# Kernel optimization log

Hardware: AMD Instinct MI355X
Metric: run time of the kernel (lower is better)

Reference implementation:

```python
import jax, jax.numpy as jnp
import numpy as np

B, F, T, K = 32, 256, 2048, 1024


def setup_inputs() -> dict:
    key = jax.random.key(0)
    k1, k2 = jax.random.split(key)
    x = jax.random.normal(k1, (B, F, T), dtype=jnp.float32)
    emb_weight = jax.random.normal(k2, (K, F), dtype=jnp.float32)
    return {"x": x, "emb_weight": emb_weight}


def reference(x, emb_weight):
    # x: [B, F, T] -> [B, T, F]
    xt = jnp.swapaxes(x, -1, -2)
    nf = xt.shape[-1]

    def sq_dist(a, c):
        # mean over feature dim of (a - c)^2, expanded to avoid a [B,T,K,F]
        # broadcast tensor: (|a|^2 - 2 a.c + |c|^2) / F -> [B, T, K]
        a2 = jnp.sum(a * a, axis=-1, keepdims=True)          # [B,T,1]
        c2 = jnp.sum(c * c, axis=-1)                          # [K]
        ac = jnp.einsum('btf,kf->btk', a, c)                  # [B,T,K]
        return (a2 - 2.0 * ac + c2) / nf

    w_sg = jax.lax.stop_gradient(emb_weight)
    x_sg = jax.lax.stop_gradient(xt)

    dist = sq_dist(xt, w_sg)                                  # [B,T,K]
    min_dist = jnp.min(dist, axis=-1)                         # [B,T]
    idxs = jnpp_argmin(dist) if False else jnp.argmin(dist, axis=-1)  # [B,T]

    loss_commit = min_dist.mean()                              # grads -> x only
    loss_codebook = jnp.min(sq_dist(x_sg, emb_weight), axis=-1).mean()  # grads -> codebook only

    out = w_sg[idxs]                                           # [B,T,F] gather (detached)
    out = jnp.swapaxes(out, -1, -2)                            # [B,F,T]
    return out, loss_commit, loss_codebook
```

## Files before the change

### kernel.cpp

```cpp
#include <hip/hip_runtime.h>

#define B_ 32
#define F_ 256
#define T_ 2048
#define K_ 1024
#define M_ (B_*T_)

#define MARGIN 0.45f
#define CAP 128

typedef _Float16 f16x8 __attribute__((ext_vector_type(8)));
typedef float f32x4 __attribute__((ext_vector_type(4)));

__global__ void k_prep(const float* __restrict__ emb, unsigned short* __restrict__ cprep,
                       double* __restrict__ c2d, float* __restrict__ c2f) {
    int k = blockIdx.x;
    int l = threadIdx.x;
    float4 v = *reinterpret_cast<const float4*>(emb + k * F_ + l * 4);
    union { _Float16 h[4]; unsigned long long ll; } cv;
    cv.h[0] = (_Float16)v.x; cv.h[1] = (_Float16)v.y;
    cv.h[2] = (_Float16)v.z; cv.h[3] = (_Float16)v.w;
    *reinterpret_cast<unsigned long long*>(cprep + k * F_ + l * 4) = cv.ll;
    double s = (double)v.x * v.x + (double)v.y * v.y
             + (double)v.z * v.z + (double)v.w * v.w;
    #pragma unroll
    for (int d = 1; d < 64; d <<= 1) s += __shfl_xor(s, d);
    if (l == 0) { c2d[k] = s; c2f[k] = (float)s; }
}

#define LOADB(dst, c2n, tt) {                                                    \
    const unsigned short* bp = cprep + ((tt) * 16 + row) * F_ + qd * 8;          \
    _Pragma("unroll")                                                            \
    for (int s_ = 0; s_ < 8; ++s_)                                               \
        dst[s_] = *reinterpret_cast<const f16x8*>(bp + s_ * 32);                 \
    c2n = c2f[(tt) * 16 + row];                                                  \
}

#define COMPUTE(bf, c2v, tt) {                                                   \
    const int kk = (tt) * 16 + row;                                              \
    f32x4 acc0 = {0.f, 0.f, 0.f, 0.f};                                           \
    f32x4 acc1 = {0.f, 0.f, 0.f, 0.f};                                           \
    _Pragma("unroll")                                                            \
    for (int s_ = 0; s_ < 8; ++s_) {                                             \
        acc0 = __builtin_amdgcn_mfma_f32_16x16x32_f16(ah0[s_], bf[s_], acc0, 0, 0, 0); \
        acc1 = __builtin_amdgcn_mfma_f32_16x16x32_f16(ah1[s_], bf[s_], acc1, 0, 0, 0); \
    }                                                                            \
    _Pragma("unroll")                                                            \
    for (int r_ = 0; r_ < 4; ++r_) {                                             \
        {                                                                        \
            float q = fmaf(acc0[r_], -2.0f, c2v + a2s[r_]);                      \
            int vi = (__float_as_int(q) & 0xFFFFFC00) | kk;                      \
            int t1 = max(m1i[r_], vi); m1i[r_] = min(m1i[r_], vi);               \
            int t2 = max(m2i[r_], t1); m2i[r_] = min(m2i[r_], t1);               \
            m3i[r_] = min(m3i[r_], t2);                                          \
        }                                                                        \
        {                                                                        \
            float q = fmaf(acc1[r_], -2.0f, c2v + a2s[4 + r_]);                  \
            int vi = (__float_as_int(q) & 0xFFFFFC00) | kk;                      \
            int t1 = max(m1i[4 + r_], vi); m1i[4 + r_] = min(m1i[4 + r_], vi);   \
            int t2 = max(m2i[4 + r_], t1); m2i[4 + r_] = min(m2i[4 + r_], t1);   \
            m3i[4 + r_] = min(m3i[4 + r_], t2);                                  \
        }                                                                        \
    }                                                                            \
}

__global__ __launch_bounds__(64, 2) void k_argmin(
    const float* __restrict__ x, const float* __restrict__ emb,
    const unsigned short* __restrict__ cprep,
    const double* __restrict__ c2d, const float* __restrict__ c2f,
    int* __restrict__ idx_out, double* __restrict__ partials)
{
    __shared__ int cand_cnt;
    __shared__ int cand_pk[CAP];
    __shared__ double cand_q[CAP];
    __shared__ int res_k[32];

    const int l = threadIdx.x;
    const int bid = blockIdx.x;
    const int b = bid >> 6;
    const int t0 = (bid & 63) * 32;
    const int row = l & 15;
    const int qd = l >> 4;

    if (l == 0) cand_cnt = 0;

    const float* xb = x + (size_t)b * (F_ * T_) + t0 + row + (size_t)qd * 8 * T_;
    float xsql = 0.f, xsqh = 0.f;
    f16x8 ah0[8], ah1[8];
    #pragma unroll
    for (int s = 0; s < 8; ++s) {
        #pragma unroll
        for (int j = 0; j < 8; ++j) {
            size_t fo = (size_t)(s * 32 + j) * T_;
            float v0 = xb[fo];
            float v1 = xb[fo + 16];
            ah0[s][j] = (_Float16)v0;
            ah1[s][j] = (_Float16)v1;
            xsql = fmaf(v0, v0, xsql);
            xsqh = fmaf(v1, v1, xsqh);
        }
    }
    float xl = xsql, xh = xsqh;
    xl += __shfl_xor(xl, 16); xl += __shfl_xor(xl, 32);
    xh += __shfl_xor(xh, 16); xh += __shfl_xor(xh, 32);
    float a2s[8];
    #pragma unroll
    for (int r = 0; r < 4; ++r) {
        a2s[r]     = __shfl(xl, qd * 4 + r);
        a2s[4 + r] = __shfl(xh, qd * 4 + r);
    }

    int m1i[8], m2i[8], m3i[8];
    #pragma unroll
    for (int i = 0; i < 8; ++i) { m1i[i] = 0x7FFFFFFF; m2i[i] = 0x7FFFFFFF; m3i[i] = 0x7FFFFFFF; }

    f16x8 bA[8], bB[8];
    float c2A, c2B;
    LOADB(bA, c2A, 0);
    #pragma unroll 1
    for (int t = 0; t < 64; t += 2) {
        LOADB(bB, c2B, t + 1);
        COMPUTE(bA, c2A, t);
        if (t + 2 < 64) LOADB(bA, c2A, t + 2);
        COMPUTE(bB, c2B, t + 1);
    }

    double loss_acc = 0.0;
    #pragma unroll
    for (int i = 0; i < 8; ++i) {
        int gm = m1i[i];
        #pragma unroll
        for (int d = 1; d < 16; d <<= 1) { int o = __shfl_xor(gm, d); gm = min(gm, o); }
        float thr = __int_as_float(gm & 0xFFFFFC00) + MARGIN;
        bool in1 = __int_as_float(m1i[i] & 0xFFFFFC00) <= thr;
        bool in2 = __int_as_float(m2i[i] & 0xFFFFFC00) <= thr;
        bool in3 = __int_as_float(m3i[i] & 0xFFFFFC00) <= thr;
        unsigned long long b1 = __ballot(in1), b2 = __ballot(in2), b3 = __ballot(in3);
        int sh = l & 48;
        int cnt = __popcll((b1 >> sh) & 0xFFFFull) + __popcll((b2 >> sh) & 0xFFFFull)
                + __popcll((b3 >> sh) & 0xFFFFull);
        int p = (i >> 2) * 16 + qd * 4 + (i & 3);
        if ((l & 15) == 0) {
            res_k[p] = gm & 1023;
            loss_acc += (double)__int_as_float((gm & 0xFFFFFC00) | 512);
        }
        if (cnt >= 2) {
            if (in1) { int s_ = atomicAdd(&cand_cnt, 1); if (s_ < CAP) cand_pk[s_] = (p << 10) | (m1i[i] & 1023); }
            if (in2) { int s_ = atomicAdd(&cand_cnt, 1); if (s_ < CAP) cand_pk[s_] = (p << 10) | (m2i[i] & 1023); }
            if (in3) { int s_ = atomicAdd(&cand_cnt, 1); if (s_ < CAP) cand_pk[s_] = (p << 10) | (m3i[i] & 1023); }
        }
    }
    __syncthreads();

    int total = cand_cnt; if (total > CAP) total = CAP;
    for (int ci = 0; ci < total; ++ci) {
        int pk = cand_pk[ci];
        int p = pk >> 10, k = pk & 1023;
        const float* xp = x + (size_t)b * (F_ * T_) + t0 + p;
        const float4 ev = *reinterpret_cast<const float4*>(emb + k * F_ + l * 4);
        double s = 0.0;
        s += (double)xp[(size_t)(l * 4 + 0) * T_] * (double)ev.x;
        s += (double)xp[(size_t)(l * 4 + 1) * T_] * (double)ev.y;
        s += (double)xp[(size_t)(l * 4 + 2) * T_] * (double)ev.z;
        s += (double)xp[(size_t)(l * 4 + 3) * T_] * (double)ev.w;
        #pragma unroll
        for (int d = 1; d < 64; d <<= 1) s += __shfl_xor(s, d);
        if (l == 0) cand_q[ci] = c2d[k] - 2.0 * s;
    }
    __syncthreads();

    if (l < 32) {
        double bq = 1e300; int bk = -1; bool any = false;
        for (int ci = 0; ci < total; ++ci) {
            int pk = cand_pk[ci];
            if ((pk >> 10) == l) {
                double q = cand_q[ci]; int k = pk & 1023;
                if (q < bq || (q == bq && k < bk)) { bq = q; bk = k; }
                any = true;
            }
        }
        idx_out[b * T_ + t0 + l] = any ? bk : res_k[l];
    }

    #pragma unroll
    for (int d = 1; d < 64; d <<= 1) loss_acc += __shfl_xor(loss_acc, d);
    if (l == 0) partials[bid] = loss_acc;
}

__global__ void k_loss(const double* __restrict__ partials, float* __restrict__ out_losses) {
    __shared__ double redd[256];
    int tid = threadIdx.x;
    double s = 0.0;
    #pragma unroll
    for (int i = 0; i < 8; ++i) s += partials[tid + i * 256];
    redd[tid] = s;
    __syncthreads();
    for (int st = 128; st > 0; st >>= 1) {
        if (tid < st) redd[tid] += redd[tid + st];
        __syncthreads();
    }
    if (tid == 0) {
        float loss = (float)(redd[0] / ((double)F_ * (double)M_));
        out_losses[0] = loss;
        out_losses[1] = loss;
    }
}

__global__ __launch_bounds__(256) void k_gather(
    const float* __restrict__ emb, const int* __restrict__ idx,
    float* __restrict__ out)
{
    __shared__ float tile[32][257];
    __shared__ int karr[32];

    const int tid = threadIdx.x;
    const int bid = blockIdx.x;
    const int b = bid >> 6;
    const int t0 = (bid & 63) * 32;

    if (tid < 32) karr[tid] = idx[b * T_ + t0 + tid];
    __syncthreads();

    #pragma unroll
    for (int pass = 0; pass < 8; ++pass) {
        int r = pass * 4 + (tid >> 6);
        int c = (tid & 63) * 4;
        *reinterpret_cast<float4*>(&tile[r][c]) =
            *reinterpret_cast<const float4*>(emb + karr[r] * F_ + c);
    }
    __syncthreads();

    #pragma unroll
    for (int pass = 0; pass < 8; ++pass) {
        int f = pass * 32 + (tid >> 3);
        int t4 = (tid & 7) * 4;
        float4 v;
        v.x = tile[t4 + 0][f];
        v.y = tile[t4 + 1][f];
        v.z = tile[t4 + 2][f];
        v.w = tile[t4 + 3][f];
        *reinterpret_cast<float4*>(out + ((size_t)b * F_ + f) * T_ + t0 + t4) = v;
    }
}

extern "C" void kernel_launch(void* const* d_in, const int* in_sizes, int n_in,
                              void* d_out, int out_size, void* d_ws, size_t ws_size,
                              hipStream_t stream) {
    const float* x   = (const float*)d_in[0];
    const float* emb = (const float*)d_in[1];
    float* out = (float*)d_out;

    double* c2d = (double*)d_ws;
    double* partials = c2d + K_;
    unsigned short* cprep = (unsigned short*)(partials + 2048);
    float* c2f = (float*)(cprep + K_ * F_);
    int* idx = (int*)(c2f + K_);

    k_prep<<<K_, 64, 0, stream>>>(emb, cprep, c2d, c2f);
    k_argmin<<<M_ / 32, 64, 0, stream>>>(x, emb, cprep, c2d, c2f, idx, partials);
    k_loss<<<1, 256, 0, stream>>>(partials, out + (size_t)M_ * F_);
    k_gather<<<M_ / 32, 256, 0, stream>>>(emb, idx, out);
}
```

Baseline: 244.9 us.

## Split codebook scan across four waves per block with shared-memory min merge

Each block now runs 256 threads (four wavefronts), and each wave scans a quarter of the codebook tiles for the same 32 rows instead of one wave scanning all 64 tiles. Per-wave top-3 minima are merged through shared memory to form a global threshold and candidate counts, and the fp64 candidate refinement is spread across the waves. This shortens the serial per-block chain and adds intra-block parallelism. The cost is that every wave redundantly loads and converts the same x tile, and extra syncthreads and shared-memory traffic are added.

```diff
diff --git a/kernel.cpp b/kernel.cpp
--- a/kernel.cpp
+++ b/kernel.cpp
@@ -64,7 +64,7 @@
     }                                                                            \
 }
 
-__global__ __launch_bounds__(64, 2) void k_argmin(
+__global__ __launch_bounds__(256, 4) void k_argmin(
     const float* __restrict__ x, const float* __restrict__ emb,
     const unsigned short* __restrict__ cprep,
     const double* __restrict__ c2d, const float* __restrict__ c2f,
@@ -73,16 +73,19 @@
     __shared__ int cand_cnt;
     __shared__ int cand_pk[CAP];
     __shared__ double cand_q[CAP];
-    __shared__ int res_k[32];
-
-    const int l = threadIdx.x;
+    __shared__ int gmw[4 * 32];
+    __shared__ int cntw[4 * 32];
+
+    const int tid = threadIdx.x;
     const int bid = blockIdx.x;
     const int b = bid >> 6;
     const int t0 = (bid & 63) * 32;
+    const int w = tid >> 6;
+    const int l = tid & 63;
     const int row = l & 15;
     const int qd = l >> 4;
 
-    if (l == 0) cand_cnt = 0;
+    if (tid == 0) cand_cnt = 0;
 
     const float* xb = x + (size_t)b * (F_ * T_) + t0 + row + (size_t)qd * 8 * T_;
     float xsql = 0.f, xsqh = 0.f;
@@ -114,24 +117,34 @@
     #pragma unroll
     for (int i = 0; i < 8; ++i) { m1i[i] = 0x7FFFFFFF; m2i[i] = 0x7FFFFFFF; m3i[i] = 0x7FFFFFFF; }
 
+    const int tbase = w * 16;
     f16x8 bA[8], bB[8];
     float c2A, c2B;
-    LOADB(bA, c2A, 0);
+    LOADB(bA, c2A, tbase);
     #pragma unroll 1
-    for (int t = 0; t < 64; t += 2) {
-        LOADB(bB, c2B, t + 1);
-        COMPUTE(bA, c2A, t);
-        if (t + 2 < 64) LOADB(bA, c2A, t + 2);
-        COMPUTE(bB, c2B, t + 1);
-    }
-
-    double loss_acc = 0.0;
+    for (int t = 0; t < 16; t += 2) {
+        LOADB(bB, c2B, tbase + t + 1);
+        COMPUTE(bA, c2A, tbase + t);
+        if (t + 2 < 16) LOADB(bA, c2A, tbase + t + 2);
+        COMPUTE(bB, c2B, tbase + t + 1);
+    }
+
     #pragma unroll
     for (int i = 0; i < 8; ++i) {
         int gm = m1i[i];
         #pragma unroll
         for (int d = 1; d < 16; d <<= 1) { int o = __shfl_xor(gm, d); gm = min(gm, o); }
-        float thr = __int_as_float(gm & 0xFFFFFC00) + MARGIN;
+        int p = (i >> 2) * 16 + qd * 4 + (i & 3);
+        if ((l & 15) == 0) gmw[w * 32 + p] = gm;
+    }
+    __syncthreads();
+
+    int inm = 0;
+    #pragma unroll
+    for (int i = 0; i < 8; ++i) {
+        int p = (i >> 2) * 16 + qd * 4 + (i & 3);
+        int gall = min(min(gmw[p], gmw[32 + p]), min(gmw[64 + p], gmw[96 + p]));
+        float thr = __int_as_float(gall & 0xFFFFFC00) + MARGIN;
         bool in1 = __int_as_float(m1i[i] & 0xFFFFFC00) <= thr;
         bool in2 = __int_as_float(m2i[i] & 0xFFFFFC00) <= thr;
         bool in3 = __int_as_float(m3i[i] & 0xFFFFFC00) <= thr;
@@ -139,21 +152,26 @@
         int sh = l & 48;
         int cnt = __popcll((b1 >> sh) & 0xFFFFull) + __popcll((b2 >> sh) & 0xFFFFull)
                 + __popcll((b3 >> sh) & 0xFFFFull);
+        if ((l & 15) == 0) cntw[w * 32 + p] = cnt;
+        inm |= ((in1 ? 1 : 0) | (in2 ? 2 : 0) | (in3 ? 4 : 0)) << (i * 3);
+    }
+    __syncthreads();
+
+    #pragma unroll
+    for (int i = 0; i < 8; ++i) {
         int p = (i >> 2) * 16 + qd * 4 + (i & 3);
-        if ((l & 15) == 0) {
-            res_k[p] = gm & 1023;
-            loss_acc += (double)__int_as_float((gm & 0xFFFFFC00) | 512);
+        int total_c = cntw[p] + cntw[32 + p] + cntw[64 + p] + cntw[96 + p];
+        if (total_c >= 2) {
+            int bits = (inm >> (i * 3)) & 7;
+            if (bits & 1) { int s_ = atomicAdd(&cand_cnt, 1); if (s_ < CAP) cand_pk[s_] = (p << 10) | (m1i[i] & 1023); }
+            if (bits & 2) { int s_ = atomicAdd(&cand_cnt, 1); if (s_ < CAP) cand_pk[s_] = (p << 10) | (m2i[i] & 1023); }
+            if (bits & 4) { int s_ = atomicAdd(&cand_cnt, 1); if (s_ < CAP) cand_pk[s_] = (p << 10) | (m3i[i] & 1023); }
         }
-        if (cnt >= 2) {
-            if (in1) { int s_ = atomicAdd(&cand_cnt, 1); if (s_ < CAP) cand_pk[s_] = (p << 10) | (m1i[i] & 1023); }
-            if (in2) { int s_ = atomicAdd(&cand_cnt, 1); if (s_ < CAP) cand_pk[s_] = (p << 10) | (m2i[i] & 1023); }
-            if (in3) { int s_ = atomicAdd(&cand_cnt, 1); if (s_ < CAP) cand_pk[s_] = (p << 10) | (m3i[i] & 1023); }
-        }
     }
     __syncthreads();
 
     int total = cand_cnt; if (total > CAP) total = CAP;
-    for (int ci = 0; ci < total; ++ci) {
+    for (int ci = w; ci < total; ci += 4) {
         int pk = cand_pk[ci];
         int p = pk >> 10, k = pk & 1023;
         const float* xp = x + (size_t)b * (F_ * T_) + t0 + p;
@@ -169,22 +187,24 @@
     }
     __syncthreads();
 
-    if (l < 32) {
+    if (tid < 32) {
+        int p = tid;
+        int gall = min(min(gmw[p], gmw[32 + p]), min(gmw[64 + p], gmw[96 + p]));
         double bq = 1e300; int bk = -1; bool any = false;
         for (int ci = 0; ci < total; ++ci) {
             int pk = cand_pk[ci];
-            if ((pk >> 10) == l) {
+            if ((pk >> 10) == p) {
                 double q = cand_q[ci]; int k = pk & 1023;
                 if (q < bq || (q == bq && k < bk)) { bq = q; bk = k; }
                 any = true;
             }
         }
-        idx_out[b * T_ + t0 + l] = any ? bk : res_k[l];
-    }
-
-    #pragma unroll
-    for (int d = 1; d < 64; d <<= 1) loss_acc += __shfl_xor(loss_acc, d);
-    if (l == 0) partials[bid] = loss_acc;
+        idx_out[b * T_ + t0 + p] = any ? bk : (gall & 1023);
+        double lossd = (double)__int_as_float((gall & 0xFFFFFC00) | 512);
+        #pragma unroll
+        for (int d = 1; d < 32; d <<= 1) lossd += __shfl_xor(lossd, d);
+        if (p == 0) partials[bid] = lossd;
+    }
 }
 
 __global__ void k_loss(const double* __restrict__ partials, float* __restrict__ out_losses) {
@@ -257,7 +277,7 @@
     int* idx = (int*)(c2f + K_);
 
     k_prep<<<K_, 64, 0, stream>>>(emb, cprep, c2d, c2f);
-    k_argmin<<<M_ / 32, 64, 0, stream>>>(x, emb, cprep, c2d, c2f, idx, partials);
+    k_argmin<<<M_ / 32, 256, 0, stream>>>(x, emb, cprep, c2d, c2f, idx, partials);
     k_loss<<<1, 256, 0, stream>>>(partials, out + (size_t)M_ * F_);
     k_gather<<<M_ / 32, 256, 0, stream>>>(emb, idx, out);
 }
```

After: 529.5 us. 2.16x slower.
